# Performance work log

Measured on AMD Instinct MI355X. Metric: run time of the kernel, lower is better.

Reference implementation:

```python
import math
import jax, jax.numpy as jnp
import numpy as np

L, B, S, D, HID, NH = 4, 2, 2048, 1024, 1024, 16
C = HID // NH  # 64


def setup_inputs() -> dict:
    key = jax.random.key(0)
    ks = jax.random.split(key, 8)
    p = lambda k, shape: jax.random.normal(k, shape, jnp.float32) * 0.02
    return {
        "x": jax.random.normal(ks[0], (B, S, D), jnp.float32),
        "Wq": p(ks[1], (L, D, HID)), "bq": jnp.zeros((L, HID), jnp.float32),
        "Wk": p(ks[2], (L, D, HID)), "bk": jnp.zeros((L, HID), jnp.float32),
        "Wv": p(ks[3], (L, D, HID)), "bv": jnp.zeros((L, HID), jnp.float32),
        "Wo": p(ks[4], (L, HID, D)), "bo": jnp.zeros((L, D), jnp.float32),
        "W1": p(ks[5], (L, D, HID)), "b1": jnp.zeros((L, HID), jnp.float32),
        "W2": p(ks[6], (L, HID, D)), "b2": jnp.zeros((L, D), jnp.float32),
        "gamma": jnp.ones((L, D), jnp.float32),   # single LayerNorm reused twice per block
        "beta": jnp.zeros((L, D), jnp.float32),
    }


def _pos_enc(seq_len, d, n=1000.0):
    col = jnp.arange(seq_len, dtype=jnp.float32)[:, None]        # [S,1]
    row = jnp.arange(d)                                          # [D]
    exp = (2.0 * (row // 2).astype(jnp.float32)) / d
    mat = col / jnp.power(n, exp)[None, :]                       # [S,D]
    return jnp.where(row % 2 == 0, jnp.sin(mat), jnp.cos(mat))


def _layernorm(x, g, b, eps=1e-5):
    mu = jnp.mean(x, axis=-1, keepdims=True)
    var = jnp.mean((x - mu) ** 2, axis=-1, keepdims=True)        # biased, as torch
    return (x - mu) / jnp.sqrt(var + eps) * g + b


def _block(x, Wq, bq, Wk, bk, Wv, bv, Wo, bo, W1, b1, W2, b2, g, be):
    b_, s_, _ = x.shape
    q = ((x @ Wq + bq)).reshape(b_, s_, NH, C) / math.sqrt(C)
    k = (x @ Wk + bk).reshape(b_, s_, NH, C)
    v = (x @ Wv + bv).reshape(b_, s_, NH, C)
    # NOTE: faithful to original einsum '...hq,...hk->...hqk' -> per-token
    # attention over the CHANNEL axis c, with a (c,c) causal mask.
    aff = jnp.einsum('bshq,bshk->bshqk', q, k)                   # [B,S,H,C,C]
    mask = jnp.triu(jnp.ones((C, C), bool), 1)
    aff = jnp.where(mask, -jnp.inf, aff)
    w = jax.nn.softmax(aff, axis=-1)
    av = jnp.einsum('bshqk,bshk->bshq', w, v).reshape(b_, s_, HID)
    attn_out = av @ Wo + bo
    x = _layernorm(attn_out + x, g, be)
    mlp_out = jax.nn.relu(x @ W1 + b1) @ W2 + b2
    return _layernorm(mlp_out + x, g, be)


def reference(x, Wq, bq, Wk, bk, Wv, bv, Wo, bo, W1, b1, W2, b2, gamma, beta):
    x = x + _pos_enc(x.shape[1], x.shape[2])
    for i in range(L):
        x = _block(x, Wq[i], bq[i], Wk[i], bk[i], Wv[i], bv[i], Wo[i], bo[i],
                   W1[i], b1[i], W2[i], b2[i], gamma[i], beta[i])
    return x
```

## Files before the change

### kernel.cpp

```cpp
#include <hip/hip_runtime.h>
#include <hip/hip_bf16.h>
#include <stdint.h>

#define TOK 4096
#define DM  1024

using u16 = unsigned short;
typedef __attribute__((ext_vector_type(8))) short short8;
typedef __attribute__((ext_vector_type(4))) float f32x4;

__device__ __forceinline__ u16 f2bf(float f){
  unsigned u = __float_as_uint(f);
  return (u16)((u + 0x7fffu + ((u >> 16) & 1u)) >> 16);
}
__device__ __forceinline__ float bf2f(u16 h){ return __uint_as_float(((unsigned)h) << 16); }

__device__ __forceinline__ float fexp2(float x){
#if __has_builtin(__builtin_amdgcn_exp2f)
  return __builtin_amdgcn_exp2f(x);
#else
  float r; asm("v_exp_f32 %0, %1\n\ts_nop 0" : "=v"(r) : "v"(x)); return r;
#endif
}
__device__ __forceinline__ float frcp(float x){
#if __has_builtin(__builtin_amdgcn_rcpf)
  return __builtin_amdgcn_rcpf(x);
#else
  float r; asm("v_rcp_f32 %0, %1\n\ts_nop 0" : "=v"(r) : "v"(x)); return r;
#endif
}

__global__ __launch_bounds__(256) void posenc_add(
    const float* __restrict__ x, u16* __restrict__ xb)
{
  const int t = blockIdx.x;
  const int s = t & 2047;
  const size_t base = (size_t)t * DM;
#pragma unroll
  for (int i = 0; i < 4; ++i){
    const int d = threadIdx.x + i * 256;
    const float e = (float)(d & ~1) * (1.0f / (float)DM);
    const float denom = powf(1000.0f, e);
    const float mat = (float)s / denom;
    const float pe = (d & 1) ? cosf(mat) : sinf(mat);
    xb[base + d] = f2bf(x[base + d] + pe);
  }
}

__global__ __launch_bounds__(256) void transpose6(
    const float* __restrict__ Wq, const float* __restrict__ Wk, const float* __restrict__ Wv,
    const float* __restrict__ Wo, const float* __restrict__ W1, const float* __restrict__ W2,
    u16* __restrict__ WT, int l0)
{
  __shared__ float tile[64 * 65];
  const int bid = blockIdx.x;
  const int l   = l0 + bid / 1536;
  const int rem = bid % 1536;
  const int mm  = rem >> 8;
  const int t   = rem & 255;
  const int tn  = (t & 15) * 64;
  const int tk  = (t >> 4) * 64;
  const float* src = (mm==0)?Wq:(mm==1)?Wk:(mm==2)?Wv:(mm==3)?Wo:(mm==4)?W1:W2;
  src += (size_t)l * 1048576;
  u16* dst = WT + ((size_t)(l - l0) * 6 + mm) * 1048576;
  const int tx = threadIdx.x & 15, ty = threadIdx.x >> 4;
#pragma unroll
  for (int r = 0; r < 4; ++r){
    const int row = ty + 16 * r;
    const float4 v = *(const float4*)(src + (size_t)(tk + row) * 1024 + tn + 4 * tx);
    tile[(4*tx + 0) * 65 + row] = v.x;
    tile[(4*tx + 1) * 65 + row] = v.y;
    tile[(4*tx + 2) * 65 + row] = v.z;
    tile[(4*tx + 3) * 65 + row] = v.w;
  }
  __syncthreads();
#pragma unroll
  for (int r = 0; r < 4; ++r){
    const int nrow = ty + 16 * r;
    ushort4 o;
    o.x = f2bf(tile[nrow * 65 + 4*tx + 0]);
    o.y = f2bf(tile[nrow * 65 + 4*tx + 1]);
    o.z = f2bf(tile[nrow * 65 + 4*tx + 2]);
    o.w = f2bf(tile[nrow * 65 + 4*tx + 3]);
    *(ushort4*)(dst + (size_t)(tn + nrow) * 1024 + tk + 4 * tx) = o;
  }
}

#define BM 128
#define BK 64
#define KD 1024

#define QBM 256
#define QBN 192
#define QNT (KD/BK)

__global__ __launch_bounds__(512, 2) void qkv_gemm8(
    const u16* __restrict__ A, const u16* __restrict__ BT,
    const float* __restrict__ bq, const float* __restrict__ bk, const float* __restrict__ bvp,
    u16* __restrict__ outB)
{
  __shared__ __align__(16) u16 lds[2][(QBM + QBN) * BK];
  const int tid  = threadIdx.x;
  const int lane = tid & 63;
  const int wave = tid >> 6;
  const int nwg  = gridDim.x;
  const int wg   = (blockIdx.x & 7) * (nwg >> 3) + (blockIdx.x >> 3);
  const int nbn  = 3072 / QBN;
  const size_t m0 = (size_t)(wg / nbn) * QBM;
  const size_t n0 = (size_t)(wg % nbn) * QBN;

  const int srow  = lane >> 3;
  const int sslot = (lane & 7) ^ srow;
  const u16* gA = A  + (m0 + wave*32 + srow) * KD + sslot * 8;
  const u16* gB = BT + (n0 + wave*24 + srow) * KD + sslot * 8;
  const int loA = wave * 32 * 64;
  const int loB = QBM * BK + wave * 24 * 64;

  auto stage1 = [&](int kt, int buf, int i){
    const int k0 = kt * BK;
    if (i < 4)
      __builtin_amdgcn_global_load_lds(
          (const __attribute__((address_space(1))) void*)(gA + i*8*KD + k0),
          (__attribute__((address_space(3))) void*)(&lds[buf][loA + i*512]), 16, 0, 0);
    else
      __builtin_amdgcn_global_load_lds(
          (const __attribute__((address_space(1))) void*)(gB + (i-4)*8*KD + k0),
          (__attribute__((address_space(3))) void*)(&lds[buf][loB + (i-4)*512]), 16, 0, 0);
  };

  const int wr = wave >> 2;
  const int wc = wave & 3;
  f32x4 acc[8][3] = {};
  short8 bfv[3][2];

#pragma unroll
  for (int i = 0; i < 7; ++i) stage1(0, 0, i);

  for (int kt = 0; kt < QNT; ++kt){
    const int cur = kt & 1;
    asm volatile("s_waitcnt vmcnt(0)" ::: "memory");
    __builtin_amdgcn_sched_barrier(0);
    __builtin_amdgcn_s_barrier();
    const u16* sA = &lds[cur][0];
    const u16* sB = &lds[cur][QBM * BK];
#pragma unroll
    for (int p = 0; p < 4; ++p){
      short8 af[2][2];
#pragma unroll
      for (int i = 0; i < 2; ++i)
#pragma unroll
        for (int kh = 0; kh < 2; ++kh){
          const int ar = wr*128 + (p*2 + i)*16 + (lane & 15);
          af[i][kh] = *(const short8*)(sA + ar*64 + ((((kh<<2)|(lane>>4)) ^ (ar & 7)) * 8));
        }
      if (p == 0){
#pragma unroll
        for (int j = 0; j < 3; ++j)
#pragma unroll
          for (int kh = 0; kh < 2; ++kh){
            const int br = wc*48 + j*16 + (lane & 15);
            bfv[j][kh] = *(const short8*)(sB + br*64 + ((((kh<<2)|(lane>>4)) ^ (br & 7)) * 8));
          }
      }
      if (kt + 1 < QNT){
        stage1(kt + 1, cur ^ 1, p*2);
        if (p*2 + 1 < 7) stage1(kt + 1, cur ^ 1, p*2 + 1);
      }
      __builtin_amdgcn_s_barrier();
      asm volatile("s_waitcnt lgkmcnt(0)" ::: "memory");
      __builtin_amdgcn_sched_barrier(0);
      __builtin_amdgcn_s_setprio(1);
#pragma unroll
      for (int i = 0; i < 2; ++i)
#pragma unroll
        for (int j = 0; j < 3; ++j)
#pragma unroll
          for (int kh = 0; kh < 2; ++kh)
            acc[p*2 + i][j] = __builtin_amdgcn_mfma_f32_16x16x32_bf16(
                af[i][kh], bfv[j][kh], acc[p*2 + i][j], 0, 0, 0);
      __builtin_amdgcn_s_setprio(0);
      __builtin_amdgcn_s_barrier();
    }
  }

#pragma unroll
  for (int m = 0; m < 8; ++m){
    const int growb = wr*128 + m*16 + (lane >> 4) * 4;
#pragma unroll
    for (int j = 0; j < 3; ++j){
      const size_t gcol = n0 + wc*48 + j*16 + (lane & 15);
      float bias;
      if (gcol < 1024)      bias = bq[gcol];
      else if (gcol < 2048) bias = bk[gcol - 1024];
      else                  bias = bvp[gcol - 2048];
#pragma unroll
      for (int r = 0; r < 4; ++r){
        const size_t grow = m0 + growb + r;
        float v = acc[m][j][r] + bias;
        if (gcol < 1024) v *= 0.125f;
        outB[grow * 3072 + gcol] = f2bf(v);
      }
    }
  }
}

template<int MODE>
__global__ __launch_bounds__(256, 3) void gemm_k1024(
    const u16* __restrict__ A, const u16* __restrict__ BT,
    const float* __restrict__ bias0,
    u16* __restrict__ outB, int M, int N)
{
  constexpr int BNt = 64;
  constexpr int NFR = 2;
  __shared__ __align__(16) u16 lds2[2][(BM + BNt) * BK];
  const int tid  = threadIdx.x;
  const int lane = tid & 63;
  const int wave = tid >> 6;
  const int nbn = N / BNt;
  const int nwg = gridDim.x;
  const int wg  = (blockIdx.x & 7) * (nwg >> 3) + (blockIdx.x >> 3);
  const size_t m0 = (size_t)(wg / nbn) * BM;
  const size_t n0 = (size_t)(wg % nbn) * BNt;

  const int srow  = lane >> 3;
  const int sslot = (lane & 7) ^ srow;
  const u16* gA = A  + (m0 + wave*32 + srow) * KD + sslot * 8;
  const u16* gB = BT + (n0 + wave*16 + srow) * KD + sslot * 8;
  const int loA = (wave*32) * 64;
  const int loB = BM*BK + (wave*16) * 64;

  const int wm = (wave >> 1) * 64;
  const int wn = (wave & 1) * 32;
  f32x4 acc[4][NFR] = {};

  auto stage = [&](int kt, int buf){
    u16* base = lds2[buf];
    const int k0 = kt * BK;
#pragma unroll
    for (int p = 0; p < 4; ++p)
      __builtin_amdgcn_global_load_lds(
          (const __attribute__((address_space(1))) void*)(gA + p*8*KD + k0),
          (__attribute__((address_space(3))) void*)(base + loA + p*512), 16, 0, 0);
#pragma unroll
    for (int p = 0; p < 2; ++p)
      __builtin_amdgcn_global_load_lds(
          (const __attribute__((address_space(1))) void*)(gB + p*8*KD + k0),
          (__attribute__((address_space(3))) void*)(base + loB + p*512), 16, 0, 0);
  };
  auto compute = [&](int buf){
    const u16* sAc = lds2[buf];
    const u16* sBc = sAc + BM*BK;
#pragma unroll
    for (int kk = 0; kk < 2; ++kk){
      short8 af[4], bfr[NFR];
      const int kidx = kk*4 + (lane >> 4);
#pragma unroll
      for (int i = 0; i < 4; ++i){
        const int arow = wm + i*16 + (lane & 15);
        af[i]  = *(const short8*)(sAc + arow*64 + (kidx ^ (arow & 7)) * 8);
      }
#pragma unroll
      for (int j = 0; j < NFR; ++j){
        const int brow = wn + j*16 + (lane & 15);
        bfr[j] = *(const short8*)(sBc + brow*64 + (kidx ^ (brow & 7)) * 8);
      }
#pragma unroll
      for (int i = 0; i < 4; ++i)
#pragma unroll
        for (int j = 0; j < NFR; ++j)
          acc[i][j] = __builtin_amdgcn_mfma_f32_16x16x32_bf16(af[i], bfr[j], acc[i][j], 0, 0, 0);
    }
  };

  stage(0, 0);
  __syncthreads();
  for (int kt = 0; kt < KD/BK; ++kt){
    if (kt + 1 < KD/BK) stage(kt + 1, (kt + 1) & 1);
    compute(kt & 1);
    __syncthreads();
  }

#pragma unroll
  for (int i = 0; i < 4; ++i){
    const int growb = wm + i*16 + (lane >> 4) * 4;
#pragma unroll
    for (int j = 0; j < NFR; ++j){
      const size_t gcol = n0 + wn + j*16 + (lane & 15);
      const float bv = bias0[gcol];
#pragma unroll
      for (int r = 0; r < 4; ++r){
        const size_t grow = m0 + growb + r;
        float v = acc[i][j][r] + bv;
        if constexpr (MODE == 1) v = fmaxf(v, 0.0f);
        outB[grow * N + gcol] = f2bf(v);
      }
    }
  }
}

__global__ __launch_bounds__(256) void attn_chan(
    const u16* __restrict__ qkv, u16* __restrict__ av)
{
  __shared__ __align__(16) float2 skv[4][2][64];
  const int t    = blockIdx.x >> 1;
  const int lane = threadIdx.x & 63;
  const int wave = threadIdx.x >> 6;
  const int h0   = (blockIdx.x & 1) * 8 + wave * 2;
  const int r3   = lane & 3;
  const size_t base = (size_t)t * 3072 + h0 * 64 + lane;
  const float q0 = bf2f(qkv[base])      * 1.44269504f;
  const float q1 = bf2f(qkv[base + 64]) * 1.44269504f;
  skv[wave][0][lane] = make_float2(bf2f(qkv[base + 1024]), bf2f(qkv[base + 2048]));
  skv[wave][1][lane] = make_float2(bf2f(qkv[base + 1088]), bf2f(qkv[base + 2112]));
  const float2* kwa = skv[wave][0];
  const float2* kwb = skv[wave][1];
  float sa0=0.f, sa1=0.f, aa0=0.f, aa1=0.f;
  float sb0=0.f, sb1=0.f, ab0=0.f, ab1=0.f;
#pragma unroll
  for (int j0 = 0; j0 < 64; j0 += 4){
    const float4 A0 = *(const float4*)(kwa + j0);
    const float4 A1 = *(const float4*)(kwa + j0 + 2);
    const float4 B0 = *(const float4*)(kwb + j0);
    const float4 B1 = *(const float4*)(kwb + j0 + 2);
    const float bias = (j0 + 3 <= lane) ? 0.0f : -200.0f;
    const float ea0 = fexp2(fmaf(q0, A0.x, bias));
    const float ea1 = fexp2(fmaf(q0, A0.z, bias));
    const float ea2 = fexp2(fmaf(q0, A1.x, bias));
    const float ea3 = fexp2(fmaf(q0, A1.z, bias));
    const float eb0 = fexp2(fmaf(q1, B0.x, bias));
    const float eb1 = fexp2(fmaf(q1, B0.z, bias));
    const float eb2 = fexp2(fmaf(q1, B1.x, bias));
    const float eb3 = fexp2(fmaf(q1, B1.z, bias));
    sa0 += ea0 + ea2;  sa1 += ea1 + ea3;
    sb0 += eb0 + eb2;  sb1 += eb1 + eb3;
    aa0 = fmaf(ea0, A0.y, fmaf(ea2, A1.y, aa0));
    aa1 = fmaf(ea1, A0.w, fmaf(ea3, A1.w, aa1));
    ab0 = fmaf(eb0, B0.y, fmaf(eb2, B1.y, ab0));
    ab1 = fmaf(eb1, B0.w, fmaf(eb3, B1.w, ab1));
  }
#pragma unroll
  for (int s = 0; s < 3; ++s){
    const int jj = lane - r3 + s;
    const float bias = (s <= r3 && r3 < 3) ? 0.0f : -200.0f;
    const float2 ka = kwa[jj];
    const float2 kb = kwb[jj];
    const float ea = fexp2(fmaf(q0, ka.x, bias));
    const float eb = fexp2(fmaf(q1, kb.x, bias));
    sa0 += ea; aa0 = fmaf(ea, ka.y, aa0);
    sb0 += eb; ab0 = fmaf(eb, kb.y, ab0);
  }
  av[(size_t)t * DM + h0*64 + lane]      = f2bf((aa0 + aa1) * frcp(sa0 + sa1));
  av[(size_t)t * DM + h0*64 + 64 + lane] = f2bf((ab0 + ab1) * frcp(sb0 + sb1));
}

__global__ __launch_bounds__(256) void residual_ln(
    const u16* __restrict__ y, const u16* xres,
    const float* __restrict__ gamma, const float* __restrict__ beta,
    float* xoutF, u16* xb)
{
  const int lane = threadIdx.x & 63, wave = threadIdx.x >> 6;
  const int row  = blockIdx.x * 4 + wave;
  const ushort4* yr = (const ushort4*)(y    + (size_t)row*DM);
  const ushort4* xr = (const ushort4*)(xres + (size_t)row*DM);
  float4 s[4];
  float psum = 0.0f;
#pragma unroll
  for (int c = 0; c < 4; ++c){
    const int idx = c*64 + lane;
    const ushort4 a = yr[idx];
    const ushort4 b = xr[idx];
    s[c].x = bf2f(a.x)+bf2f(b.x); s[c].y = bf2f(a.y)+bf2f(b.y);
    s[c].z = bf2f(a.z)+bf2f(b.z); s[c].w = bf2f(a.w)+bf2f(b.w);
    psum += (s[c].x + s[c].y) + (s[c].z + s[c].w);
  }
#pragma unroll
  for (int o = 32; o; o >>= 1) psum += __shfl_xor(psum, o);
  const float mu = psum * (1.0f/(float)DM);
  float q2 = 0.0f;
#pragma unroll
  for (int c = 0; c < 4; ++c){
    s[c].x -= mu; s[c].y -= mu; s[c].z -= mu; s[c].w -= mu;
    q2 += s[c].x*s[c].x + s[c].y*s[c].y + s[c].z*s[c].z + s[c].w*s[c].w;
  }
#pragma unroll
  for (int o = 32; o; o >>= 1) q2 += __shfl_xor(q2, o);
  const float rstd = rsqrtf(q2 * (1.0f/(float)DM) + 1e-5f);
#pragma unroll
  for (int c = 0; c < 4; ++c){
    const int idx = c*64 + lane;
    const float4 g  = ((const float4*)gamma)[idx];
    const float4 be = ((const float4*)beta)[idx];
    float4 o4;
    o4.x = s[c].x*rstd*g.x + be.x;
    o4.y = s[c].y*rstd*g.y + be.y;
    o4.z = s[c].z*rstd*g.z + be.z;
    o4.w = s[c].w*rstd*g.w + be.w;
    if (xoutF) ((float4*)(xoutF + (size_t)row*DM))[idx] = o4;
    ushort4 ob; ob.x=f2bf(o4.x); ob.y=f2bf(o4.y); ob.z=f2bf(o4.z); ob.w=f2bf(o4.w);
    ((ushort4*)(xb + (size_t)row*DM))[idx] = ob;
  }
}

extern "C" void kernel_launch(void* const* d_in, const int* in_sizes, int n_in,
                              void* d_out, int out_size, void* d_ws, size_t ws_size,
                              hipStream_t stream)
{
  const float* x    = (const float*)d_in[0];
  const float* Wq   = (const float*)d_in[1];
  const float* bq   = (const float*)d_in[2];
  const float* Wk   = (const float*)d_in[3];
  const float* bk   = (const float*)d_in[4];
  const float* Wv   = (const float*)d_in[5];
  const float* bv   = (const float*)d_in[6];
  const float* Wo   = (const float*)d_in[7];
  const float* bo   = (const float*)d_in[8];
  const float* W1   = (const float*)d_in[9];
  const float* b1   = (const float*)d_in[10];
  const float* W2   = (const float*)d_in[11];
  const float* b2   = (const float*)d_in[12];
  const float* gam  = (const float*)d_in[13];
  const float* bet  = (const float*)d_in[14];

  char* ws = (char*)d_ws;
  size_t off = 0;
  auto alloc = [&](size_t b){ void* p = ws + off; off = (off + b + 255) & ~(size_t)255; return p; };

  const size_t oneWT = 6ull*1048576*2;
  const size_t rest  = ((size_t)TOK*DM*2)
                     + ((size_t)TOK*3072*2)
                     + ((size_t)TOK*DM*2)
                     + ((size_t)TOK*DM*2)
                     + ((size_t)TOK*DM*2)
                     + 4096;
  const bool all4 = (4*oneWT + rest) <= ws_size;

  u16*   WT   = (u16*)  alloc(all4 ? 4*oneWT : oneWT);
  u16*   xb   = (u16*)  alloc((size_t)TOK*DM*2);
  u16*   qkv  = (u16*)  alloc((size_t)TOK*3072*2);
  u16*   avb  = (u16*)  alloc((size_t)TOK*DM*2);
  u16*   hbuf = (u16*)  alloc((size_t)TOK*DM*2);
  u16*   ybuf = (u16*)  alloc((size_t)TOK*DM*2);
  if (off > ws_size) return;

  posenc_add<<<TOK, 256, 0, stream>>>(x, xb);
  if (all4)
    transpose6<<<4*1536, 256, 0, stream>>>(Wq, Wk, Wv, Wo, W1, W2, WT, 0);

  for (int l = 0; l < 4; ++l){
    u16* wt = all4 ? (WT + (size_t)l * 6 * 1048576) : WT;
    if (!all4)
      transpose6<<<1536, 256, 0, stream>>>(Wq, Wk, Wv, Wo, W1, W2, WT, l);
    qkv_gemm8<<<(TOK/QBM)*(3072/QBN), 512, 0, stream>>>(
        xb, wt, bq + l*1024, bk + l*1024, bv + l*1024, qkv);
    attn_chan<<<TOK*2, 256, 0, stream>>>(qkv, avb);
    gemm_k1024<0><<<(TOK/BM)*(1024/64), 256, 0, stream>>>(
        avb, wt + 3ull*1048576, bo + l*1024, ybuf, TOK, 1024);
    residual_ln<<<TOK/4, 256, 0, stream>>>(ybuf, xb, gam + l*1024, bet + l*1024, nullptr, xb);
    gemm_k1024<1><<<(TOK/BM)*(1024/64), 256, 0, stream>>>(
        xb, wt + 4ull*1048576, b1 + l*1024, hbuf, TOK, 1024);
    gemm_k1024<0><<<(TOK/BM)*(1024/64), 256, 0, stream>>>(
        hbuf, wt + 5ull*1048576, b2 + l*1024, ybuf, TOK, 1024);
    residual_ln<<<TOK/4, 256, 0, stream>>>(ybuf, xb, gam + l*1024, bet + l*1024,
                                           (l == 3) ? (float*)d_out : nullptr, xb);
  }
}
```

Baseline: 536.2 us.

## Replace N=1024 GEMMs with 8-wave 256x64 tile kernel and interleaved prefetch

Replaces the 4-wave 128x64-tile GEMM used for the output projection and both MLP layers with an 8-wave 256x64-tile kernel. Global-to-LDS loads for the next K tile are issued in pieces between the LDS fragment reads and the MFMA bursts of the current tile. B fragments are read once per K tile and reused across two A sub-steps, and MFMA sections run at raised wave priority. The launch grid halves to 256 workgroups, which adds reuse of the A operand but gives fewer blocks and more barriers per K step.

```diff
diff --git a/kernel.cpp b/kernel.cpp
--- a/kernel.cpp
+++ b/kernel.cpp
@@ -86,7 +86,6 @@
   }
 }
 
-#define BM 128
 #define BK 64
 #define KD 1024
 
@@ -204,95 +203,111 @@
   }
 }
 
+#define SBM 256
+#define SBN 64
+
 template<int MODE>
-__global__ __launch_bounds__(256, 3) void gemm_k1024(
+__global__ __launch_bounds__(512, 2) void gemm8_n1024(
     const u16* __restrict__ A, const u16* __restrict__ BT,
-    const float* __restrict__ bias0,
-    u16* __restrict__ outB, int M, int N)
-{
-  constexpr int BNt = 64;
-  constexpr int NFR = 2;
-  __shared__ __align__(16) u16 lds2[2][(BM + BNt) * BK];
+    const float* __restrict__ bias0, u16* __restrict__ outB)
+{
+  __shared__ __align__(16) u16 lds[2][(SBM + SBN) * BK];
   const int tid  = threadIdx.x;
   const int lane = tid & 63;
   const int wave = tid >> 6;
-  const int nbn = N / BNt;
-  const int nwg = gridDim.x;
-  const int wg  = (blockIdx.x & 7) * (nwg >> 3) + (blockIdx.x >> 3);
-  const size_t m0 = (size_t)(wg / nbn) * BM;
-  const size_t n0 = (size_t)(wg % nbn) * BNt;
+  const int nwg  = gridDim.x;
+  const int wg   = (blockIdx.x & 7) * (nwg >> 3) + (blockIdx.x >> 3);
+  const size_t m0 = (size_t)(wg >> 4) * SBM;
+  const size_t n0 = (size_t)(wg & 15) * SBN;
 
   const int srow  = lane >> 3;
   const int sslot = (lane & 7) ^ srow;
   const u16* gA = A  + (m0 + wave*32 + srow) * KD + sslot * 8;
-  const u16* gB = BT + (n0 + wave*16 + srow) * KD + sslot * 8;
-  const int loA = (wave*32) * 64;
-  const int loB = BM*BK + (wave*16) * 64;
-
-  const int wm = (wave >> 1) * 64;
-  const int wn = (wave & 1) * 32;
-  f32x4 acc[4][NFR] = {};
-
-  auto stage = [&](int kt, int buf){
-    u16* base = lds2[buf];
+  const u16* gB = BT + (n0 + wave*8  + srow) * KD + sslot * 8;
+  const int loA = wave * 32 * 64;
+  const int loB = SBM * BK + wave * 8 * 64;
+
+  auto stage1 = [&](int kt, int buf, int i){
     const int k0 = kt * BK;
-#pragma unroll
-    for (int p = 0; p < 4; ++p)
+    if (i < 4)
       __builtin_amdgcn_global_load_lds(
-          (const __attribute__((address_space(1))) void*)(gA + p*8*KD + k0),
-          (__attribute__((address_space(3))) void*)(base + loA + p*512), 16, 0, 0);
-#pragma unroll
-    for (int p = 0; p < 2; ++p)
+          (const __attribute__((address_space(1))) void*)(gA + i*8*KD + k0),
+          (__attribute__((address_space(3))) void*)(&lds[buf][loA + i*512]), 16, 0, 0);
+    else
       __builtin_amdgcn_global_load_lds(
-          (const __attribute__((address_space(1))) void*)(gB + p*8*KD + k0),
-          (__attribute__((address_space(3))) void*)(base + loB + p*512), 16, 0, 0);
+          (const __attribute__((address_space(1))) void*)(gB + k0),
+          (__attribute__((address_space(3))) void*)(&lds[buf][loB]), 16, 0, 0);
   };
-  auto compute = [&](int buf){
-    const u16* sAc = lds2[buf];
-    const u16* sBc = sAc + BM*BK;
-#pragma unroll
-    for (int kk = 0; kk < 2; ++kk){
-      short8 af[4], bfr[NFR];
-      const int kidx = kk*4 + (lane >> 4);
-#pragma unroll
-      for (int i = 0; i < 4; ++i){
-        const int arow = wm + i*16 + (lane & 15);
-        af[i]  = *(const short8*)(sAc + arow*64 + (kidx ^ (arow & 7)) * 8);
-      }
-#pragma unroll
-      for (int j = 0; j < NFR; ++j){
-        const int brow = wn + j*16 + (lane & 15);
-        bfr[j] = *(const short8*)(sBc + brow*64 + (kidx ^ (brow & 7)) * 8);
-      }
-#pragma unroll
-      for (int i = 0; i < 4; ++i)
-#pragma unroll
-        for (int j = 0; j < NFR; ++j)
-          acc[i][j] = __builtin_amdgcn_mfma_f32_16x16x32_bf16(af[i], bfr[j], acc[i][j], 0, 0, 0);
+
+  const int wr = wave >> 1;
+  const int wc = wave & 1;
+  f32x4 acc[4][2] = {};
+  short8 bfv[2][2];
+
+#pragma unroll
+  for (int i = 0; i < 5; ++i) stage1(0, 0, i);
+
+  for (int kt = 0; kt < KD/BK; ++kt){
+    const int cur = kt & 1;
+    asm volatile("s_waitcnt vmcnt(0)" ::: "memory");
+    __builtin_amdgcn_sched_barrier(0);
+    __builtin_amdgcn_s_barrier();
+    const u16* sA = &lds[cur][0];
+    const u16* sB = &lds[cur][SBM * BK];
+#pragma unroll
+    for (int p = 0; p < 2; ++p){
+      short8 af[2][2];
+#pragma unroll
+      for (int i = 0; i < 2; ++i)
+#pragma unroll
+        for (int kh = 0; kh < 2; ++kh){
+          const int ar = wr*64 + (p*2 + i)*16 + (lane & 15);
+          af[i][kh] = *(const short8*)(sA + ar*64 + ((((kh<<2)|(lane>>4)) ^ (ar & 7)) * 8));
+        }
+      if (p == 0){
+#pragma unroll
+        for (int j = 0; j < 2; ++j)
+#pragma unroll
+          for (int kh = 0; kh < 2; ++kh){
+            const int br = wc*32 + j*16 + (lane & 15);
+            bfv[j][kh] = *(const short8*)(sB + br*64 + ((((kh<<2)|(lane>>4)) ^ (br & 7)) * 8));
+          }
+      }
+      if (kt + 1 < KD/BK){
+        stage1(kt + 1, cur ^ 1, p*3);
+        stage1(kt + 1, cur ^ 1, p*3 + 1);
+        if (p == 0) stage1(kt + 1, cur ^ 1, 2);
+      }
+      __builtin_amdgcn_s_barrier();
+      asm volatile("s_waitcnt lgkmcnt(0)" ::: "memory");
+      __builtin_amdgcn_sched_barrier(0);
+      __builtin_amdgcn_s_setprio(1);
+#pragma unroll
+      for (int i = 0; i < 2; ++i)
+#pragma unroll
+        for (int j = 0; j < 2; ++j)
+#pragma unroll
+          for (int kh = 0; kh < 2; ++kh)
+            acc[p*2 + i][j] = __builtin_amdgcn_mfma_f32_16x16x32_bf16(
+                af[i][kh], bfv[j][kh], acc[p*2 + i][j], 0, 0, 0);
+      __builtin_amdgcn_s_setprio(0);
+      __builtin_amdgcn_s_barrier();
     }
-  };
-
-  stage(0, 0);
-  __syncthreads();
-  for (int kt = 0; kt < KD/BK; ++kt){
-    if (kt + 1 < KD/BK) stage(kt + 1, (kt + 1) & 1);
-    compute(kt & 1);
-    __syncthreads();
-  }
-
-#pragma unroll
-  for (int i = 0; i < 4; ++i){
-    const int growb = wm + i*16 + (lane >> 4) * 4;
-#pragma unroll
-    for (int j = 0; j < NFR; ++j){
-      const size_t gcol = n0 + wn + j*16 + (lane & 15);
+  }
+
+#pragma unroll
+  for (int m = 0; m < 4; ++m){
+    const int growb = wr*64 + m*16 + (lane >> 4) * 4;
+#pragma unroll
+    for (int j = 0; j < 2; ++j){
+      const size_t gcol = n0 + wc*32 + j*16 + (lane & 15);
       const float bv = bias0[gcol];
 #pragma unroll
       for (int r = 0; r < 4; ++r){
         const size_t grow = m0 + growb + r;
-        float v = acc[i][j][r] + bv;
+        float v = acc[m][j][r] + bv;
         if constexpr (MODE == 1) v = fmaxf(v, 0.0f);
-        outB[grow * N + gcol] = f2bf(v);
+        outB[grow * 1024 + gcol] = f2bf(v);
       }
     }
   }
@@ -453,13 +468,13 @@
     qkv_gemm8<<<(TOK/QBM)*(3072/QBN), 512, 0, stream>>>(
         xb, wt, bq + l*1024, bk + l*1024, bv + l*1024, qkv);
     attn_chan<<<TOK*2, 256, 0, stream>>>(qkv, avb);
-    gemm_k1024<0><<<(TOK/BM)*(1024/64), 256, 0, stream>>>(
-        avb, wt + 3ull*1048576, bo + l*1024, ybuf, TOK, 1024);
+    gemm8_n1024<0><<<(TOK/SBM)*(1024/SBN), 512, 0, stream>>>(
+        avb, wt + 3ull*1048576, bo + l*1024, ybuf);
     residual_ln<<<TOK/4, 256, 0, stream>>>(ybuf, xb, gam + l*1024, bet + l*1024, nullptr, xb);
-    gemm_k1024<1><<<(TOK/BM)*(1024/64), 256, 0, stream>>>(
-        xb, wt + 4ull*1048576, b1 + l*1024, hbuf, TOK, 1024);
-    gemm_k1024<0><<<(TOK/BM)*(1024/64), 256, 0, stream>>>(
-        hbuf, wt + 5ull*1048576, b2 + l*1024, ybuf, TOK, 1024);
+    gemm8_n1024<1><<<(TOK/SBM)*(1024/SBN), 512, 0, stream>>>(
+        xb, wt + 4ull*1048576, b1 + l*1024, hbuf);
+    gemm8_n1024<0><<<(TOK/SBM)*(1024/SBN), 512, 0, stream>>>(
+        hbuf, wt + 5ull*1048576, b2 + l*1024, ybuf);
     residual_ln<<<TOK/4, 256, 0, stream>>>(ybuf, xb, gam + l*1024, bet + l*1024,
                                            (l == 3) ? (float*)d_out : nullptr, xb);
   }
```

After: 566.0 us. 5.6% more time.
